# Kernel tuning notes

Hardware: AMD Instinct MI355X
Metric: run time of the kernel (lower is better)

Reference implementation:

```python
import jax, jax.numpy as jnp
import numpy as np

B, N, K = 8, 4096, 20          # clouds, points per cloud, knn neighbors
IN_C, OUT_C = 3, 64            # xyz coords -> feature channels


def setup_inputs() -> dict:
    key = jax.random.key(0)
    k1, k2 = jax.random.split(key, 2)
    x = jax.random.normal(k1, (B * N, IN_C), dtype=jnp.float32)
    batch = (jnp.arange(B * N, dtype=jnp.int32) // N)  # [0..0,1..1,...] equal-size clouds
    # EdgeConv MLP: Linear(2*in_channels -> out_channels) + ReLU
    W = jax.random.normal(k2, (2 * IN_C, OUT_C), dtype=jnp.float32) / jnp.sqrt(jnp.float32(2 * IN_C))
    b = jnp.zeros((OUT_C,), dtype=jnp.float32)
    return {"x": x, "batch": batch, "W": W, "b": b}


def _knn_idx(xr):
    # xr: [B, N, C] -> neighbor indices [B, N, K] (self excluded, like knn_graph loop=False)
    sq = jnp.sum(xr * xr, axis=-1)                                  # [B, N]
    d = sq[:, :, None] + sq[:, None, :] - 2.0 * jnp.einsum("bnd,bmd->bnm", xr, xr)  # [B,N,N]
    ar = jnp.arange(N)
    d = d.at[:, ar, ar].set(jnp.inf)                                 # exclude self-loops
    _, idx = jax.lax.top_k(-d, K)                                    # k smallest distances
    return idx


def reference(x, batch, W, b):
    # batch encodes B equal-size clouds of N points each (constant structure)
    xr = x.reshape(B, N, IN_C)
    idx = _knn_idx(xr)                                               # [B, N, K]
    x_j = jax.vmap(lambda pts, i: pts[i])(xr, idx)                   # gather neighbors [B,N,K,C]
    x_i = xr[:, :, None, :]                                          # center points   [B,N,1,C]
    msg = jnp.concatenate([jnp.broadcast_to(x_i, x_j.shape), x_j - x_i], axis=-1)  # [B,N,K,2C]
    h = jax.nn.relu(jnp.einsum("bnkc,co->bnko", msg, W) + b)         # EdgeConv MLP
    out = jnp.max(h, axis=2)                                         # max aggregation over K
    return out.reshape(B * N, OUT_C)
```

## Files before the change

### kernel.cpp

```cpp
#include <hip/hip_runtime.h>
#include <math.h>

#define NN    4096
#define KK    20
#define QQ    4
#define WAVES 4
#define BLK   (WAVES*64)
#define PPB   (WAVES*QQ)
#define IPT   (NN/64)
#define CAP   56
#define BPB   (NN/PPB)
#define BB    8

__device__ __forceinline__ unsigned fkey(float f) {
  unsigned u = __float_as_uint(f);
  return u ^ ((unsigned)((int)u >> 31) | 0x80000000u);
}
__device__ __forceinline__ float fkey_inv(unsigned k) {
  unsigned u = (k & 0x80000000u) ? (k ^ 0x80000000u) : ~k;
  return __uint_as_float(u);
}

__global__ void prep_kernel(const float* __restrict__ x, float4* __restrict__ ws4) {
  const int i = blockIdx.x * 256 + threadIdx.x;
  const float* p = x + (size_t)i * 3;
  const float a = p[0], b = p[1], c = p[2];
  ws4[i] = make_float4(a, b, c, fmaf(c, c, fmaf(b, b, a * a)));
}

template<bool WS>
__global__ __launch_bounds__(BLK, 8)
void edgeconv_kernel(const float* __restrict__ x,
                     const float4* __restrict__ ws4,
                     const float* __restrict__ W,
                     const float* __restrict__ bias,
                     float* __restrict__ out) {
  __shared__ float2 cand[PPB][CAP + 1];
  __shared__ int    jkeep[PPB][21];
  __shared__ int    pc[PPB];
  __shared__ int    pk[PPB];

  const int tid  = threadIdx.x;
  const int lane = tid & 63;
  const int w    = tid >> 6;
  const int bb   = blockIdx.x / BPB;
  const int blk  = blockIdx.x % BPB;
  const int base = bb * NN;
  const int g0   = w * QQ;
  const int myp0 = blk * PPB + g0;

  float nx[QQ], ny[QQ], nz[QQ];
  #pragma unroll
  for (int q = 0; q < QQ; ++q) {
    const float* p = x + (size_t)(base + myp0 + q) * 3;
    nx[q] = -2.f * p[0]; ny[q] = -2.f * p[1]; nz[q] = -2.f * p[2];
  }

  if (tid < PPB) { pc[tid] = 0; pk[tid] = 0; }
  __syncthreads();

  auto ldp = [&](int j) -> float4 {
    if constexpr (WS) {
      return ws4[base + j];
    } else {
      const float* p = x + (size_t)(base + j) * 3;
      const float a = p[0], b = p[1], c = p[2];
      return make_float4(a, b, c, fmaf(c, c, fmaf(b, b, a * a)));
    }
  };

  float m[QQ];
  #pragma unroll
  for (int q = 0; q < QQ; ++q) m[q] = INFINITY;
  #pragma unroll 1
  for (int i = 0; i < IPT; i += 4) {
    const float4 v0 = ldp((i + 0) * 64 + lane);
    const float4 v1 = ldp((i + 1) * 64 + lane);
    const float4 v2 = ldp((i + 2) * 64 + lane);
    const float4 v3 = ldp((i + 3) * 64 + lane);
    #pragma unroll
    for (int q = 0; q < QQ; ++q) {
      const float d0 = fmaf(nx[q], v0.x, fmaf(ny[q], v0.y, fmaf(nz[q], v0.z, v0.w)));
      const float d1 = fmaf(nx[q], v1.x, fmaf(ny[q], v1.y, fmaf(nz[q], v1.z, v1.w)));
      const float d2 = fmaf(nx[q], v2.x, fmaf(ny[q], v2.y, fmaf(nz[q], v2.z, v2.w)));
      const float d3 = fmaf(nx[q], v3.x, fmaf(ny[q], v3.y, fmaf(nz[q], v3.z, v3.w)));
      m[q] = fminf(fminf(fminf(fminf(m[q], d0), d1), d2), d3);
    }
  }

  float tau[QQ];
  #pragma unroll
  for (int q = 0; q < QQ; ++q) {
    const unsigned key = fkey(m[q]);
    unsigned lo = 0u, hi = 0xFFFFFFFFu;
    for (int b = 0; b < 32; ++b) {
      const unsigned mid = lo + ((hi - lo) >> 1);
      const unsigned long long bal = __ballot(key <= mid);
      if (__popcll(bal) > KK) hi = mid; else lo = mid + 1;
    }
    tau[q] = fkey_inv(lo);
  }

  #pragma unroll 1
  for (int i = 0; i < IPT; i += 4) {
    const float4 v0 = ldp((i + 0) * 64 + lane);
    const float4 v1 = ldp((i + 1) * 64 + lane);
    const float4 v2 = ldp((i + 2) * 64 + lane);
    const float4 v3 = ldp((i + 3) * 64 + lane);
    #pragma unroll
    for (int q = 0; q < QQ; ++q) {
      const float d0 = fmaf(nx[q], v0.x, fmaf(ny[q], v0.y, fmaf(nz[q], v0.z, v0.w)));
      const float d1 = fmaf(nx[q], v1.x, fmaf(ny[q], v1.y, fmaf(nz[q], v1.z, v1.w)));
      const float d2 = fmaf(nx[q], v2.x, fmaf(ny[q], v2.y, fmaf(nz[q], v2.z, v2.w)));
      const float d3 = fmaf(nx[q], v3.x, fmaf(ny[q], v3.y, fmaf(nz[q], v3.z, v3.w)));
      if (d0 <= tau[q]) { const int wp = atomicAdd(&pc[g0 + q], 1);
        if (wp < CAP) cand[g0 + q][wp] = make_float2(d0, __int_as_float((i + 0) * 64 + lane)); }
      if (d1 <= tau[q]) { const int wp = atomicAdd(&pc[g0 + q], 1);
        if (wp < CAP) cand[g0 + q][wp] = make_float2(d1, __int_as_float((i + 1) * 64 + lane)); }
      if (d2 <= tau[q]) { const int wp = atomicAdd(&pc[g0 + q], 1);
        if (wp < CAP) cand[g0 + q][wp] = make_float2(d2, __int_as_float((i + 2) * 64 + lane)); }
      if (d3 <= tau[q]) { const int wp = atomicAdd(&pc[g0 + q], 1);
        if (wp < CAP) cand[g0 + q][wp] = make_float2(d3, __int_as_float((i + 3) * 64 + lane)); }
    }
  }
  __syncthreads();

  {
    const int g   = tid >> 4;
    const int k0  = tid & 15;
    const int myp = blk * PPB + g;
    const int n0  = pc[g];
    const int n   = n0 < CAP ? n0 : CAP;
    for (int k = k0; k < n; k += 16) {
      const float2 ck = cand[g][k];
      const float dk = ck.x; const int jk = __float_as_int(ck.y);
      int rank = 0;
      for (int k2 = 0; k2 < n; ++k2) {
        const float2 c2 = cand[g][k2];
        rank += (c2.x < dk || (c2.x == dk && __float_as_int(c2.y) < jk)) ? 1 : 0;
      }
      if (jk != myp && rank <= KK) jkeep[g][atomicAdd(&pk[g], 1)] = jk;
    }
  }
  __syncthreads();

  const float w3 = W[3*64+lane], w4 = W[4*64+lane], w5 = W[5*64+lane];
  const float c0 = W[0*64+lane] - w3;
  const float c1 = W[1*64+lane] - w4;
  const float c2 = W[2*64+lane] - w5;
  const float bo = bias[lane];

  for (int pi = 0; pi < QQ; ++pi) {
    const int p   = g0 + pi;
    const int pid = blk * PPB + p;
    const float4 xi = ldp(pid);
    const float ci = fmaf(xi.x, c0, fmaf(xi.y, c1, fmaf(xi.z, c2, bo)));
    float hmax = -INFINITY;
    #pragma unroll 5
    for (int k = 0; k < KK; ++k) {
      const int j = jkeep[p][k];
      const float4 xp = ldp(j);
      hmax = fmaxf(hmax, fmaf(xp.x, w3, fmaf(xp.y, w4, fmaf(xp.z, w5, ci))));
    }
    out[(size_t)(base + pid) * 64 + lane] = fmaxf(hmax, 0.0f);
  }
}

extern "C" void kernel_launch(void* const* d_in, const int* in_sizes, int n_in,
                              void* d_out, int out_size, void* d_ws, size_t ws_size,
                              hipStream_t stream) {
  const float* x  = (const float*)d_in[0];
  const float* W  = (const float*)d_in[2];
  const float* b  = (const float*)d_in[3];
  float* out = (float*)d_out;

  const size_t need = (size_t)BB * NN * sizeof(float4);
  dim3 grid(BB * BPB);
  dim3 block(BLK);
  if (ws_size >= need) {
    float4* ws4 = (float4*)d_ws;
    hipLaunchKernelGGL(prep_kernel, dim3(BB * NN / 256), dim3(256), 0, stream, x, ws4);
    hipLaunchKernelGGL((edgeconv_kernel<true>), grid, block, 0, stream, x, ws4, W, b, out);
  } else {
    hipLaunchKernelGGL((edgeconv_kernel<false>), grid, block, 0, stream,
                       x, (const float4*)nullptr, W, b, out);
  }
}
```

Measured before the change: 85.22 us.

## Use packed FP32 FMA with paired-point SoA layout for distance scans

The prep kernel now also writes a paired layout in which each lane's two consecutive points are interleaved as {x0,x1,y0,y1},{z0,z1,w0,w1}. Both distance passes compute two candidate distances per v_pk_fma_f32 chain, which should roughly halve the VALU instruction count of the dominant brute-force scan. The workspace requirement doubles, and if the workspace is too small the fallback path takes on strided 6-float loads. Candidate indices are rebuilt from the pair index.

```diff
diff --git a/kernel.cpp b/kernel.cpp
--- a/kernel.cpp
+++ b/kernel.cpp
@@ -7,11 +7,20 @@
 #define WAVES 4
 #define BLK   (WAVES*64)
 #define PPB   (WAVES*QQ)
-#define IPT   (NN/64)
+#define IPT   (NN/128)
 #define CAP   56
 #define BPB   (NN/PPB)
 #define BB    8
 
+typedef float f32x4 __attribute__((ext_vector_type(4)));
+typedef float f32x2 __attribute__((ext_vector_type(2)));
+
+__device__ __forceinline__ f32x2 pk_fma(f32x2 a, f32x2 b, f32x2 c) {
+  f32x2 d;
+  asm("v_pk_fma_f32 %0, %1, %2, %3" : "=v"(d) : "v"(a), "v"(b), "v"(c));
+  return d;
+}
+
 __device__ __forceinline__ unsigned fkey(float f) {
   unsigned u = __float_as_uint(f);
   return u ^ ((unsigned)((int)u >> 31) | 0x80000000u);
@@ -21,17 +30,26 @@
   return __uint_as_float(u);
 }
 
-__global__ void prep_kernel(const float* __restrict__ x, float4* __restrict__ ws4) {
-  const int i = blockIdx.x * 256 + threadIdx.x;
-  const float* p = x + (size_t)i * 3;
-  const float a = p[0], b = p[1], c = p[2];
-  ws4[i] = make_float4(a, b, c, fmaf(c, c, fmaf(b, b, a * a)));
+__global__ void prep_kernel(const float* __restrict__ x,
+                            float4* __restrict__ ws4,
+                            f32x4* __restrict__ wspk) {
+  const int p = blockIdx.x * 256 + threadIdx.x;
+  const float* s = x + (size_t)p * 6;
+  const float x0 = s[0], y0 = s[1], z0 = s[2];
+  const float x1 = s[3], y1 = s[4], z1 = s[5];
+  const float w0 = fmaf(z0, z0, fmaf(y0, y0, x0 * x0));
+  const float w1 = fmaf(z1, z1, fmaf(y1, y1, x1 * x1));
+  ws4[2 * p]     = make_float4(x0, y0, z0, w0);
+  ws4[2 * p + 1] = make_float4(x1, y1, z1, w1);
+  wspk[2 * p]     = (f32x4){x0, x1, y0, y1};
+  wspk[2 * p + 1] = (f32x4){z0, z1, w0, w1};
 }
 
 template<bool WS>
 __global__ __launch_bounds__(BLK, 8)
 void edgeconv_kernel(const float* __restrict__ x,
                      const float4* __restrict__ ws4,
+                     const f32x4* __restrict__ wspk,
                      const float* __restrict__ W,
                      const float* __restrict__ bias,
                      float* __restrict__ out) {
@@ -49,16 +67,30 @@
   const int g0   = w * QQ;
   const int myp0 = blk * PPB + g0;
 
-  float nx[QQ], ny[QQ], nz[QQ];
+  f32x2 nxp[QQ], nyp[QQ], nzp[QQ];
   #pragma unroll
   for (int q = 0; q < QQ; ++q) {
     const float* p = x + (size_t)(base + myp0 + q) * 3;
-    nx[q] = -2.f * p[0]; ny[q] = -2.f * p[1]; nz[q] = -2.f * p[2];
+    const float a = -2.f * p[0], b = -2.f * p[1], c = -2.f * p[2];
+    nxp[q] = (f32x2){a, a}; nyp[q] = (f32x2){b, b}; nzp[q] = (f32x2){c, c};
   }
 
   if (tid < PPB) { pc[tid] = 0; pk[tid] = 0; }
   __syncthreads();
 
+  auto ldpair = [&](int pr, f32x4& A, f32x4& Bv) {
+    if constexpr (WS) {
+      A  = wspk[base + (pr << 1)];
+      Bv = wspk[base + (pr << 1) + 1];
+    } else {
+      const float* s = x + ((size_t)base + ((size_t)pr << 1)) * 3;
+      const float x0 = s[0], y0 = s[1], z0 = s[2];
+      const float x1 = s[3], y1 = s[4], z1 = s[5];
+      A  = (f32x4){x0, x1, y0, y1};
+      Bv = (f32x4){z0, z1, fmaf(z0, z0, fmaf(y0, y0, x0 * x0)),
+                           fmaf(z1, z1, fmaf(y1, y1, x1 * x1))};
+    }
+  };
   auto ldp = [&](int j) -> float4 {
     if constexpr (WS) {
       return ws4[base + j];
@@ -72,19 +104,16 @@
   float m[QQ];
   #pragma unroll
   for (int q = 0; q < QQ; ++q) m[q] = INFINITY;
-  #pragma unroll 1
-  for (int i = 0; i < IPT; i += 4) {
-    const float4 v0 = ldp((i + 0) * 64 + lane);
-    const float4 v1 = ldp((i + 1) * 64 + lane);
-    const float4 v2 = ldp((i + 2) * 64 + lane);
-    const float4 v3 = ldp((i + 3) * 64 + lane);
+  #pragma unroll 2
+  for (int i = 0; i < IPT; ++i) {
+    f32x4 A, Bv;
+    ldpair(i * 64 + lane, A, Bv);
     #pragma unroll
     for (int q = 0; q < QQ; ++q) {
-      const float d0 = fmaf(nx[q], v0.x, fmaf(ny[q], v0.y, fmaf(nz[q], v0.z, v0.w)));
-      const float d1 = fmaf(nx[q], v1.x, fmaf(ny[q], v1.y, fmaf(nz[q], v1.z, v1.w)));
-      const float d2 = fmaf(nx[q], v2.x, fmaf(ny[q], v2.y, fmaf(nz[q], v2.z, v2.w)));
-      const float d3 = fmaf(nx[q], v3.x, fmaf(ny[q], v3.y, fmaf(nz[q], v3.z, v3.w)));
-      m[q] = fminf(fminf(fminf(fminf(m[q], d0), d1), d2), d3);
+      const f32x2 d = pk_fma(nxp[q], A.xy,
+                       pk_fma(nyp[q], A.zw,
+                        pk_fma(nzp[q], Bv.xy, Bv.zw)));
+      m[q] = fminf(fminf(m[q], d.x), d.y);
     }
   }
 
@@ -101,26 +130,20 @@
     tau[q] = fkey_inv(lo);
   }
 
-  #pragma unroll 1
-  for (int i = 0; i < IPT; i += 4) {
-    const float4 v0 = ldp((i + 0) * 64 + lane);
-    const float4 v1 = ldp((i + 1) * 64 + lane);
-    const float4 v2 = ldp((i + 2) * 64 + lane);
-    const float4 v3 = ldp((i + 3) * 64 + lane);
+  #pragma unroll 2
+  for (int i = 0; i < IPT; ++i) {
+    f32x4 A, Bv;
+    ldpair(i * 64 + lane, A, Bv);
+    const int j0 = (i * 64 + lane) << 1;
     #pragma unroll
     for (int q = 0; q < QQ; ++q) {
-      const float d0 = fmaf(nx[q], v0.x, fmaf(ny[q], v0.y, fmaf(nz[q], v0.z, v0.w)));
-      const float d1 = fmaf(nx[q], v1.x, fmaf(ny[q], v1.y, fmaf(nz[q], v1.z, v1.w)));
-      const float d2 = fmaf(nx[q], v2.x, fmaf(ny[q], v2.y, fmaf(nz[q], v2.z, v2.w)));
-      const float d3 = fmaf(nx[q], v3.x, fmaf(ny[q], v3.y, fmaf(nz[q], v3.z, v3.w)));
-      if (d0 <= tau[q]) { const int wp = atomicAdd(&pc[g0 + q], 1);
-        if (wp < CAP) cand[g0 + q][wp] = make_float2(d0, __int_as_float((i + 0) * 64 + lane)); }
-      if (d1 <= tau[q]) { const int wp = atomicAdd(&pc[g0 + q], 1);
-        if (wp < CAP) cand[g0 + q][wp] = make_float2(d1, __int_as_float((i + 1) * 64 + lane)); }
-      if (d2 <= tau[q]) { const int wp = atomicAdd(&pc[g0 + q], 1);
-        if (wp < CAP) cand[g0 + q][wp] = make_float2(d2, __int_as_float((i + 2) * 64 + lane)); }
-      if (d3 <= tau[q]) { const int wp = atomicAdd(&pc[g0 + q], 1);
-        if (wp < CAP) cand[g0 + q][wp] = make_float2(d3, __int_as_float((i + 3) * 64 + lane)); }
+      const f32x2 d = pk_fma(nxp[q], A.xy,
+                       pk_fma(nyp[q], A.zw,
+                        pk_fma(nzp[q], Bv.xy, Bv.zw)));
+      if (d.x <= tau[q]) { const int wp = atomicAdd(&pc[g0 + q], 1);
+        if (wp < CAP) cand[g0 + q][wp] = make_float2(d.x, __int_as_float(j0)); }
+      if (d.y <= tau[q]) { const int wp = atomicAdd(&pc[g0 + q], 1);
+        if (wp < CAP) cand[g0 + q][wp] = make_float2(d.y, __int_as_float(j0 + 1)); }
     }
   }
   __syncthreads();
@@ -174,15 +197,19 @@
   const float* b  = (const float*)d_in[3];
   float* out = (float*)d_out;
 
-  const size_t need = (size_t)BB * NN * sizeof(float4);
+  const size_t aosz = (size_t)BB * NN * sizeof(float4);
+  const size_t need = 2 * aosz;
   dim3 grid(BB * BPB);
   dim3 block(BLK);
   if (ws_size >= need) {
     float4* ws4 = (float4*)d_ws;
-    hipLaunchKernelGGL(prep_kernel, dim3(BB * NN / 256), dim3(256), 0, stream, x, ws4);
-    hipLaunchKernelGGL((edgeconv_kernel<true>), grid, block, 0, stream, x, ws4, W, b, out);
+    f32x4* wspk = (f32x4*)((char*)d_ws + aosz);
+    hipLaunchKernelGGL(prep_kernel, dim3(BB * NN / 2 / 256), dim3(256), 0, stream,
+                       x, ws4, wspk);
+    hipLaunchKernelGGL((edgeconv_kernel<true>), grid, block, 0, stream,
+                       x, ws4, wspk, W, b, out);
   } else {
     hipLaunchKernelGGL((edgeconv_kernel<false>), grid, block, 0, stream,
-                       x, (const float4*)nullptr, W, b, out);
-  }
-}
+                       x, (const float4*)nullptr, (const f32x4*)nullptr, W, b, out);
+  }
+}
```

Result: slower. 92.10 us (+8.1%).

## Split candidate scan across two wave halves with eight queries per wave

Applied to the files above, without the earlier changes.

Each block now has 8 waves and 32 points; waves are paired so each half scans half of the cloud for 8 query points, doubling per-wave query reuse of each loaded point. Per-lane partial minima from both halves are combined through shared memory, and one wave computes the threshold with a two-ballot bisection before broadcasting it. This aims to cut redundant global loads per query and raise arithmetic reuse. The cost is extra barriers, serialized threshold search in half the waves, and higher register pressure from 8 queries.

```diff
diff --git a/kernel.cpp b/kernel.cpp
--- a/kernel.cpp
+++ b/kernel.cpp
@@ -3,11 +3,12 @@
 
 #define NN    4096
 #define KK    20
-#define QQ    4
-#define WAVES 4
+#define QQ    8
+#define WAVES 8
 #define BLK   (WAVES*64)
-#define PPB   (WAVES*QQ)
-#define IPT   (NN/64)
+#define PPB   32
+#define HALF  (NN/2)
+#define IPT   (HALF/64)
 #define CAP   56
 #define BPB   (NN/PPB)
 #define BB    8
@@ -35,6 +36,8 @@
                      const float* __restrict__ W,
                      const float* __restrict__ bias,
                      float* __restrict__ out) {
+  __shared__ float  fmin[4][QQ][64];
+  __shared__ float  taus[PPB];
   __shared__ float2 cand[PPB][CAP + 1];
   __shared__ int    jkeep[PPB][21];
   __shared__ int    pc[PPB];
@@ -43,11 +46,14 @@
   const int tid  = threadIdx.x;
   const int lane = tid & 63;
   const int w    = tid >> 6;
+  const int go   = w & 3;
+  const int h    = w >> 2;
+  const int g0   = go * QQ;
   const int bb   = blockIdx.x / BPB;
   const int blk  = blockIdx.x % BPB;
   const int base = bb * NN;
-  const int g0   = w * QQ;
   const int myp0 = blk * PPB + g0;
+  const int jb0  = h * HALF;
 
   float nx[QQ], ny[QQ], nz[QQ];
   #pragma unroll
@@ -55,9 +61,7 @@
     const float* p = x + (size_t)(base + myp0 + q) * 3;
     nx[q] = -2.f * p[0]; ny[q] = -2.f * p[1]; nz[q] = -2.f * p[2];
   }
-
   if (tid < PPB) { pc[tid] = 0; pk[tid] = 0; }
-  __syncthreads();
 
   auto ldp = [&](int j) -> float4 {
     if constexpr (WS) {
@@ -74,10 +78,10 @@
   for (int q = 0; q < QQ; ++q) m[q] = INFINITY;
   #pragma unroll 1
   for (int i = 0; i < IPT; i += 4) {
-    const float4 v0 = ldp((i + 0) * 64 + lane);
-    const float4 v1 = ldp((i + 1) * 64 + lane);
-    const float4 v2 = ldp((i + 2) * 64 + lane);
-    const float4 v3 = ldp((i + 3) * 64 + lane);
+    const float4 v0 = ldp(jb0 + (i + 0) * 64 + lane);
+    const float4 v1 = ldp(jb0 + (i + 1) * 64 + lane);
+    const float4 v2 = ldp(jb0 + (i + 2) * 64 + lane);
+    const float4 v3 = ldp(jb0 + (i + 3) * 64 + lane);
     #pragma unroll
     for (int q = 0; q < QQ; ++q) {
       const float d0 = fmaf(nx[q], v0.x, fmaf(ny[q], v0.y, fmaf(nz[q], v0.z, v0.w)));
@@ -88,25 +92,37 @@
     }
   }
 
+  if (h == 1) {
+    #pragma unroll
+    for (int q = 0; q < QQ; ++q) fmin[go][q][lane] = m[q];
+  }
+  __syncthreads();
+
+  if (h == 0) {
+    #pragma unroll 1
+    for (int q = 0; q < QQ; ++q) {
+      const unsigned k1 = fkey(m[q]);
+      const unsigned k2 = fkey(fmin[go][q][lane]);
+      unsigned lo = 0u, hi = 0xFFFFFFFFu;
+      for (int b = 0; b < 32; ++b) {
+        const unsigned mid = lo + ((hi - lo) >> 1);
+        const int cnt = __popcll(__ballot(k1 <= mid)) + __popcll(__ballot(k2 <= mid));
+        if (cnt > KK) hi = mid; else lo = mid + 1;
+      }
+      taus[g0 + q] = fkey_inv(lo);
+    }
+  }
+  __syncthreads();
   float tau[QQ];
   #pragma unroll
-  for (int q = 0; q < QQ; ++q) {
-    const unsigned key = fkey(m[q]);
-    unsigned lo = 0u, hi = 0xFFFFFFFFu;
-    for (int b = 0; b < 32; ++b) {
-      const unsigned mid = lo + ((hi - lo) >> 1);
-      const unsigned long long bal = __ballot(key <= mid);
-      if (__popcll(bal) > KK) hi = mid; else lo = mid + 1;
-    }
-    tau[q] = fkey_inv(lo);
-  }
+  for (int q = 0; q < QQ; ++q) tau[q] = taus[g0 + q];
 
   #pragma unroll 1
   for (int i = 0; i < IPT; i += 4) {
-    const float4 v0 = ldp((i + 0) * 64 + lane);
-    const float4 v1 = ldp((i + 1) * 64 + lane);
-    const float4 v2 = ldp((i + 2) * 64 + lane);
-    const float4 v3 = ldp((i + 3) * 64 + lane);
+    const float4 v0 = ldp(jb0 + (i + 0) * 64 + lane);
+    const float4 v1 = ldp(jb0 + (i + 1) * 64 + lane);
+    const float4 v2 = ldp(jb0 + (i + 2) * 64 + lane);
+    const float4 v3 = ldp(jb0 + (i + 3) * 64 + lane);
     #pragma unroll
     for (int q = 0; q < QQ; ++q) {
       const float d0 = fmaf(nx[q], v0.x, fmaf(ny[q], v0.y, fmaf(nz[q], v0.z, v0.w)));
@@ -114,13 +130,13 @@
       const float d2 = fmaf(nx[q], v2.x, fmaf(ny[q], v2.y, fmaf(nz[q], v2.z, v2.w)));
       const float d3 = fmaf(nx[q], v3.x, fmaf(ny[q], v3.y, fmaf(nz[q], v3.z, v3.w)));
       if (d0 <= tau[q]) { const int wp = atomicAdd(&pc[g0 + q], 1);
-        if (wp < CAP) cand[g0 + q][wp] = make_float2(d0, __int_as_float((i + 0) * 64 + lane)); }
+        if (wp < CAP) cand[g0 + q][wp] = make_float2(d0, __int_as_float(jb0 + (i + 0) * 64 + lane)); }
       if (d1 <= tau[q]) { const int wp = atomicAdd(&pc[g0 + q], 1);
-        if (wp < CAP) cand[g0 + q][wp] = make_float2(d1, __int_as_float((i + 1) * 64 + lane)); }
+        if (wp < CAP) cand[g0 + q][wp] = make_float2(d1, __int_as_float(jb0 + (i + 1) * 64 + lane)); }
       if (d2 <= tau[q]) { const int wp = atomicAdd(&pc[g0 + q], 1);
-        if (wp < CAP) cand[g0 + q][wp] = make_float2(d2, __int_as_float((i + 2) * 64 + lane)); }
+        if (wp < CAP) cand[g0 + q][wp] = make_float2(d2, __int_as_float(jb0 + (i + 2) * 64 + lane)); }
       if (d3 <= tau[q]) { const int wp = atomicAdd(&pc[g0 + q], 1);
-        if (wp < CAP) cand[g0 + q][wp] = make_float2(d3, __int_as_float((i + 3) * 64 + lane)); }
+        if (wp < CAP) cand[g0 + q][wp] = make_float2(d3, __int_as_float(jb0 + (i + 3) * 64 + lane)); }
     }
   }
   __syncthreads();
@@ -150,8 +166,8 @@
   const float c2 = W[2*64+lane] - w5;
   const float bo = bias[lane];
 
-  for (int pi = 0; pi < QQ; ++pi) {
-    const int p   = g0 + pi;
+  for (int pi = 0; pi < 4; ++pi) {
+    const int p   = w * 4 + pi;
     const int pid = blk * PPB + p;
     const float4 xi = ldp(pid);
     const float ci = fmaf(xi.x, c0, fmaf(xi.y, c1, fmaf(xi.z, c2, bo)));
```

After: 85.56 us. No clear change (+0.4%).
